# Performance work log

Hardware: AMD Instinct MI355X
Metric: run time of the kernel (lower is better)

## Reference

```python
import jax, jax.numpy as jnp
import numpy as np

EMBED_DIM = 1024
HEADS = 16
HEAD_DIM = EMBED_DIM // HEADS


def setup_inputs() -> dict:
    key = jax.random.key(0)
    ks = jax.random.split(key, 5)
    B, N, C = 2, 2048, EMBED_DIM
    scale = 1.0 / np.sqrt(C)
    x = jax.random.normal(ks[0], (B, N, C), dtype=jnp.float32)
    W_qkv = jax.random.normal(ks[1], (C, 3 * C), dtype=jnp.float32) * scale
    b_qkv = jax.random.normal(ks[2], (3 * C,), dtype=jnp.float32) * 0.01
    W_out = jax.random.normal(ks[3], (C, C), dtype=jnp.float32) * scale
    b_out = jax.random.normal(ks[4], (C,), dtype=jnp.float32) * 0.01
    return {"x": x, "W_qkv": W_qkv, "b_qkv": b_qkv, "W_out": W_out, "b_out": b_out}


def reference(x, W_qkv, b_qkv, W_out, b_out):
    B, N, C = x.shape
    qkv = x @ W_qkv + b_qkv                      # [B, N, 3C]
    qkv = qkv.reshape(B, N, 3, HEADS, HEAD_DIM)
    qkv = jnp.transpose(qkv, (2, 0, 3, 1, 4))    # [3, B, H, N, d]
    q, k, v = qkv[0], qkv[1], qkv[2]
    attn = jnp.einsum('bhnd,bhmd->bhnm', q, k) / np.sqrt(HEAD_DIM)
    attn = jax.nn.softmax(attn, axis=-1)
    out = jnp.einsum('bhnm,bhmd->bhnd', attn, v)  # [B, H, N, d]
    out = jnp.transpose(out, (0, 2, 1, 3)).reshape(B, N, C)
    return out @ W_out + b_out
```

## Files before the change

kernel.cpp:

```cpp
#include <hip/hip_runtime.h>
#include <stdint.h>

typedef __bf16 bf16_t;
typedef bf16_t bf16x8 __attribute__((ext_vector_type(8)));
typedef bf16_t bf16x2v __attribute__((ext_vector_type(2)));
typedef float f32x4 __attribute__((ext_vector_type(4)));
typedef float f32x16 __attribute__((ext_vector_type(16)));
typedef uint32_t u32x2 __attribute__((ext_vector_type(2)));
typedef uint32_t u32x4 __attribute__((ext_vector_type(4)));

#define BATCH 2
#define SEQ 2048
#define CDIM 1024
#define NH 16
#define HD 64

#define QSCALE 0.18033688011f

__device__ __forceinline__ uint16_t f32_bf16(float f) {
    __bf16 h = (__bf16)f;
    return __builtin_bit_cast(uint16_t, h);
}

__device__ __forceinline__ uint32_t pack_bf16(float a, float b) {
    bf16x2v t;
    t.x = (__bf16)a;
    t.y = (__bf16)b;
    return __builtin_bit_cast(uint32_t, t);
}

__device__ __forceinline__ bf16x8 ld8(const uint16_t* p) {
    return *reinterpret_cast<const bf16x8*>(p);
}

__device__ __forceinline__ void swap32(uint32_t& a, uint32_t& b) {
#if __has_builtin(__builtin_amdgcn_permlane32_swap)
    u32x2 r = __builtin_amdgcn_permlane32_swap(a, b, false, false);
    a = r.x;
    b = r.y;
#else
    asm("v_permlane32_swap_b32 %0, %1" : "+v"(a), "+v"(b));
#endif
}

__device__ __forceinline__ void gld16(const uint16_t* g, uint16_t* l) {
    __builtin_amdgcn_global_load_lds(
        (__attribute__((address_space(1))) void*)(g),
        (__attribute__((address_space(3))) void*)(l), 16, 0, 0);
}

#define LDS_FENCE() asm volatile("s_waitcnt lgkmcnt(0)" ::: "memory")

__global__ __launch_bounds__(256) void prep_kernel(
        const float* __restrict__ x, uint16_t* __restrict__ x_bf,
        const float* __restrict__ Wqkv, uint16_t* __restrict__ wqkvT,
        const float* __restrict__ Wout, uint16_t* __restrict__ woutT) {
    const int bid = blockIdx.x, tid = threadIdx.x;
    if (bid < 4096) {
        int i = (bid * 256 + tid) * 4;
        float4 v = *(const float4*)(x + i);
        ushort4 o;
        o.x = f32_bf16(v.x);
        o.y = f32_bf16(v.y);
        o.z = f32_bf16(v.z);
        o.w = f32_bf16(v.w);
        *(ushort4*)(x_bf + i) = o;
        return;
    }
    __shared__ float tile[32][33];
    const float* in;
    uint16_t* outp;
    int idx, Cc, ncx;
    if (bid < 4096 + 3072) { idx = bid - 4096; in = Wqkv; outp = wqkvT; Cc = 3072; ncx = 96; }
    else                   { idx = bid - 7168; in = Wout; outp = woutT; Cc = 1024; ncx = 32; }
    const int R = 1024;
    int bx = idx % ncx, by = idx / ncx;
    int c0 = bx * 32, r0 = by * 32;
    int tx = tid & 31, ty = tid >> 5;
#pragma unroll
    for (int i = 0; i < 4; i++)
        tile[ty + i * 8][tx] = in[(size_t)(r0 + ty + i * 8) * Cc + c0 + tx];
    __syncthreads();
    const int rr = tid >> 3, seg = tid & 7;
    ushort4 o;
    o.x = f32_bf16(tile[seg * 4 + 0][rr]);
    o.y = f32_bf16(tile[seg * 4 + 1][rr]);
    o.z = f32_bf16(tile[seg * 4 + 2][rr]);
    o.w = f32_bf16(tile[seg * 4 + 3][rr]);
    *(ushort4*)(outp + (size_t)(c0 + rr) * R + r0 + seg * 4) = o;
}

template <int BM, int BN, int MODE>
__global__ __launch_bounds__(256) void gemm_t(
        const uint16_t* __restrict__ A, const uint16_t* __restrict__ Bt, int K,
        const float* __restrict__ bias,
        uint16_t* __restrict__ qw, uint16_t* __restrict__ kw, uint16_t* __restrict__ vt,
        float* __restrict__ out) {
    constexpr int WT_M = BM / 2, WT_N = BN / 2;
    constexpr int MI = WT_M / 16, NJ = WT_N / 16;
    constexpr int ASEG_W = BM / 64, BSEG_W = BN / 64;
    constexpr int AB = 2 * BM * 32 + 2 * BN * 32;
    constexpr int TS = (MODE == 0) ? 4 * 64 * 68 : 0;
    constexpr int SM = AB > TS ? AB : TS;
    __shared__ uint16_t smem[SM];
    uint16_t* As = smem;
    uint16_t* Bs = smem + 2 * BM * 32;

    const int m0 = blockIdx.y * BM, n0 = blockIdx.x * BN;
    const int tid = threadIdx.x;
    const int w = tid >> 6, lane = tid & 63;
    const int quad = lane >> 4, l16 = lane & 15;
    const int wm = (w >> 1) * WT_M, wn = (w & 1) * WT_N;

    const int srow = lane >> 2;
    const int schunk = (lane & 3) ^ (srow & 3);

    const uint16_t* aP[ASEG_W];
    const uint16_t* bP[BSEG_W];
    int aL[ASEG_W], bL[BSEG_W];
#pragma unroll
    for (int s = 0; s < ASEG_W; s++) {
        int seg = w * ASEG_W + s;
        aP[s] = A + (size_t)(m0 + seg * 16 + srow) * K + schunk * 8;
        aL[s] = seg * 512;
    }
#pragma unroll
    for (int s = 0; s < BSEG_W; s++) {
        int seg = w * BSEG_W + s;
        bP[s] = Bt + (size_t)(n0 + seg * 16 + srow) * K + schunk * 8;
        bL[s] = seg * 512;
    }

    auto stage = [&](int buf, int k0) {
#pragma unroll
        for (int s = 0; s < ASEG_W; s++) gld16(aP[s] + k0, As + buf * BM * 32 + aL[s]);
#pragma unroll
        for (int s = 0; s < BSEG_W; s++) gld16(bP[s] + k0, Bs + buf * BN * 32 + bL[s]);
    };

    const int cslot = (quad ^ (l16 & 3)) * 8;
    f32x4 acc[MI][NJ] = {};

    stage(0, 0);
    const int iters = K / 32;
    for (int it = 0; it < iters; ++it) {
        __syncthreads();
        if (it + 1 < iters) stage((it + 1) & 1, (it + 1) * 32);
        const uint16_t* A_ = As + (it & 1) * BM * 32;
        const uint16_t* B_ = Bs + (it & 1) * BN * 32;
        bf16x8 af[MI], bfr[NJ];
#pragma unroll
        for (int i = 0; i < MI; i++) af[i] = ld8(&A_[(wm + i * 16 + l16) * 32 + cslot]);
#pragma unroll
        for (int j = 0; j < NJ; j++) bfr[j] = ld8(&B_[(wn + j * 16 + l16) * 32 + cslot]);
#pragma unroll
        for (int i = 0; i < MI; i++)
#pragma unroll
            for (int j = 0; j < NJ; j++)
                acc[i][j] = __builtin_amdgcn_mfma_f32_16x16x32_bf16(af[i], bfr[j], acc[i][j], 0, 0, 0);
    }

    const int nbase = n0 + wn;
    float bj[NJ];
#pragma unroll
    for (int j = 0; j < NJ; j++) bj[j] = bias[nbase + j * 16 + l16];

    if constexpr (MODE == 1) {
#pragma unroll
        for (int j = 0; j < NJ; j++) {
#pragma unroll
            for (int i = 0; i < MI; i++)
#pragma unroll
                for (int r = 0; r < 4; r++) {
                    int m = m0 + wm + i * 16 + quad * 4 + r;
                    out[(size_t)m * CDIM + nbase + j * 16 + l16] = acc[i][j][r] + bj[j];
                }
        }
    } else {
        __syncthreads();
        uint16_t* T = smem + w * 64 * 68;
        const int gmb = m0 + wm;
        const int b = gmb >> 11, ns0 = gmb & 2047;

        if (nbase < 2048) {
            const int which = nbase >> 10, h = (nbase & 1023) >> 6;
            const float sc = (which == 0) ? QSCALE : 1.0f;
#pragma unroll
            for (int i = 0; i < 4; i++)
#pragma unroll
                for (int j = 0; j < 4; j++)
#pragma unroll
                    for (int r = 0; r < 4; r++)
                        T[(i * 16 + quad * 4 + r) * 68 + j * 16 + l16] =
                            f32_bf16((acc[i][j][r] + bj[j]) * sc);
            LDS_FENCE();
            uint16_t* dst = ((which == 0) ? qw : kw) +
                            (((size_t)b * NH + h) * SEQ + ns0 + lane) * HD;
#pragma unroll
            for (int g = 0; g < 8; g++) {
                bf16x8 v = ld8(&T[lane * 68 + g * 8]);
                *(bf16x8*)(dst + g * 8) = v;
            }
        } else {
#pragma unroll
            for (int i = 0; i < 4; i++)
#pragma unroll
                for (int j = 0; j < 4; j++) {
                    u32x2 pr;
                    pr.x = pack_bf16(acc[i][j][0] + bj[j], acc[i][j][1] + bj[j]);
                    pr.y = pack_bf16(acc[i][j][2] + bj[j], acc[i][j][3] + bj[j]);
                    *(u32x2*)&T[(j * 16 + l16) * 68 + i * 16 + quad * 4] = pr;
                }
            LDS_FENCE();
            const int h = (nbase - 2048) >> 6;
            uint16_t* dst = vt + (((size_t)b * NH + h) * HD + lane) * SEQ + ns0;
#pragma unroll
            for (int g = 0; g < 16; g++) {
                u32x2 d2 = *(const u32x2*)&T[lane * 68 + g * 4];
                *(u32x2*)(dst + g * 4) = d2;
            }
        }
    }
}

__global__ __launch_bounds__(256) void attn_kernel(
        const uint16_t* __restrict__ qg, const uint16_t* __restrict__ kg,
        const uint16_t* __restrict__ vt, uint16_t* __restrict__ og) {
    __shared__ uint16_t Ks[2][128 * 64];
    __shared__ uint16_t Vs[2][64 * 128];

    const int bh = blockIdx.x;
    const int qt = blockIdx.y;
    const int tid = threadIdx.x;
    const int w = tid >> 6, lane = tid & 63;
    const int l32 = lane & 31, hi = lane >> 5;
    const int qrow0 = qt * 128 + w * 32;
    const size_t base = (size_t)bh * SEQ * HD;

    bf16x8 qf[4];
#pragma unroll
    for (int s = 0; s < 4; s++)
        qf[s] = ld8(qg + base + (size_t)(qrow0 + l32) * HD + s * 16 + hi * 8);

    const int krow = lane >> 3;
    const int kch = (lane & 7) ^ krow;
    const int vrow = lane >> 4;
    const uint16_t* ksrc[4];
    const uint16_t* vsrc[4];
#pragma unroll
    for (int s = 0; s < 4; s++) {
        int seg = w * 4 + s;
        ksrc[s] = kg + base + (size_t)(seg * 8 + krow) * HD + kch * 8;
        int vd = seg * 4 + vrow;
        int vch = (lane & 15) ^ (vd & 15);
        vsrc[s] = vt + base + (size_t)vd * SEQ + vch * 8;
    }

    f32x16 o_acc[2] = {};
    float l_red = 0.0f;

    auto stage = [&](int buf) {
#pragma unroll
        for (int s = 0; s < 4; s++) {
            int seg = w * 4 + s;
            gld16(ksrc[s], &Ks[buf][seg * 512]);
            ksrc[s] += 128 * HD;
        }
#pragma unroll
        for (int s = 0; s < 4; s++) {
            int seg = w * 4 + s;
            gld16(vsrc[s], &Vs[buf][seg * 512]);
            vsrc[s] += 128;
        }
    };

    stage(0);

    const int kxe = l32 & 7;
    const int vxe = l32 & 15;
    const int krowb = l32 * 64;
    const int vrowb = l32 * 128;
    int kco[4];
#pragma unroll
    for (int s = 0; s < 4; s++) kco[s] = ((2 * s + hi) ^ kxe) * 8;
    int vco[4][2];
#pragma unroll
    for (int kvb = 0; kvb < 4; kvb++)
#pragma unroll
        for (int cp = 0; cp < 2; cp++)
            vco[kvb][cp] = ((kvb * 4 + cp * 2 + hi) ^ vxe) * 8;

    const f32x16 fzero = {};

    const int NT = SEQ / 128;
    for (int it = 0; it < NT; ++it) {
        __syncthreads();
        if (it + 1 < NT) stage((it + 1) & 1);
        const uint16_t* K_ = Ks[it & 1];
        const uint16_t* V_ = Vs[it & 1];

        bf16x8 kf[2][4];
        f32x16 S[2];
#pragma unroll
        for (int s = 0; s < 4; s++) kf[0][s] = ld8(K_ + krowb + kco[s]);
        S[0] = fzero;
#pragma unroll
        for (int s = 0; s < 4; s++)
            S[0] = __builtin_amdgcn_mfma_f32_32x32x16_bf16(kf[0][s], qf[s], S[0], 0, 0, 0);

#pragma unroll
        for (int kvb = 0; kvb < 4; kvb++) {
            const int cur = kvb & 1, nxt = cur ^ 1;

            if (kvb < 3) {
#pragma unroll
                for (int s = 0; s < 4; s++)
                    kf[nxt][s] = ld8(K_ + (kvb + 1) * 2048 + krowb + kco[s]);
            }
            bf16x8 vf[2][2];
#pragma unroll
            for (int cp = 0; cp < 2; cp++)
#pragma unroll
                for (int mf = 0; mf < 2; mf++)
                    vf[cp][mf] = ld8(V_ + vrowb + mf * 4096 + vco[kvb][cp]);

            float p[16];
#pragma unroll
            for (int i = 0; i < 16; i++) p[i] = __builtin_amdgcn_exp2f(S[cur][i]);
            {
                float s0 = (p[0] + p[1]) + (p[2] + p[3]);
                float s1 = (p[4] + p[5]) + (p[6] + p[7]);
                float s2 = (p[8] + p[9]) + (p[10] + p[11]);
                float s3 = (p[12] + p[13]) + (p[14] + p[15]);
                l_red += (s0 + s1) + (s2 + s3);
            }
            uint32_t pk0[4], pk1[4];
#pragma unroll
            for (int c = 0; c < 4; c++) {
                pk0[c] = pack_bf16(p[4 * c + 0], p[4 * c + 1]);
                pk1[c] = pack_bf16(p[4 * c + 2], p[4 * c + 3]);
            }

            if (kvb < 3) {
                S[nxt] = fzero;
#pragma unroll
                for (int s = 0; s < 4; s++)
                    S[nxt] = __builtin_amdgcn_mfma_f32_32x32x16_bf16(kf[nxt][s], qf[s], S[nxt], 0, 0, 0);
            }

#pragma unroll
            for (int cp = 0; cp < 2; cp++) {
                uint32_t b0 = pk0[2 * cp], b2 = pk0[2 * cp + 1];
                uint32_t b1 = pk1[2 * cp], b3 = pk1[2 * cp + 1];
                swap32(b0, b2);
                swap32(b1, b3);
                u32x4 t;
                t.x = b0; t.y = b1; t.z = b2; t.w = b3;
                bf16x8 pb = __builtin_bit_cast(bf16x8, t);
#pragma unroll
                for (int mf = 0; mf < 2; mf++)
                    o_acc[mf] = __builtin_amdgcn_mfma_f32_32x32x16_bf16(vf[cp][mf], pb, o_acc[mf], 0, 0, 0);
            }
        }
    }

    uint32_t la = __builtin_bit_cast(uint32_t, l_red), lb = la;
    swap32(la, lb);
    const float l_tot = __builtin_bit_cast(float, la) + __builtin_bit_cast(float, lb);
    const float inv = __builtin_amdgcn_rcpf(l_tot);

    const int b = bh >> 4, h = bh & 15;
    const int ns = qrow0 + l32;
    uint16_t* orow = og + (((size_t)b * SEQ + ns) * NH + h) * HD;
#pragma unroll
    for (int mf = 0; mf < 2; mf++)
#pragma unroll
        for (int c = 0; c < 4; c++) {
            u32x2 pr;
            pr.x = pack_bf16(o_acc[mf][4 * c + 0] * inv, o_acc[mf][4 * c + 1] * inv);
            pr.y = pack_bf16(o_acc[mf][4 * c + 2] * inv, o_acc[mf][4 * c + 3] * inv);
            *(u32x2*)(orow + mf * 32 + c * 8 + hi * 4) = pr;
        }
}

extern "C" void kernel_launch(void* const* d_in, const int* in_sizes, int n_in,
                              void* d_out, int out_size, void* d_ws, size_t ws_size,
                              hipStream_t stream) {
    const float* x = (const float*)d_in[0];
    const float* Wqkv = (const float*)d_in[1];
    const float* bqkv = (const float*)d_in[2];
    const float* Wout = (const float*)d_in[3];
    const float* bout = (const float*)d_in[4];
    float* out = (float*)d_out;

    uint16_t* ws = (uint16_t*)d_ws;
    uint16_t* x_bf  = ws;
    uint16_t* wqkvT = x_bf + 4194304;
    uint16_t* woutT = wqkvT + 3145728;
    uint16_t* qw    = woutT + 1048576;
    uint16_t* kw    = qw + 4194304;
    uint16_t* vtw   = kw + 4194304;
    uint16_t* attn  = vtw + 4194304;

    prep_kernel<<<8192, 256, 0, stream>>>(x, x_bf, Wqkv, wqkvT, Wout, woutT);

    gemm_t<128, 128, 0><<<dim3(24, 32), 256, 0, stream>>>(
        x_bf, wqkvT, 1024, bqkv, qw, kw, vtw, nullptr);

    attn_kernel<<<dim3(32, 16), 256, 0, stream>>>(qw, kw, vtw, attn);

    gemm_t<64, 128, 1><<<dim3(8, 64), 256, 0, stream>>>(
        attn, woutT, 1024, bout, nullptr, nullptr, nullptr, out);
}
```

Measured before the change: 183.6 us.

## Pipeline QK^T across KV tiles via global K prefetch and coalesce QKV stores

The attention loop now computes the first S block of the next KV tile during the current tile's last sub-block. It reads those K fragments straight from global memory, so the per-tile pipeline bubble after each barrier goes away. MFMA sections are wrapped in s_setprio to favour matrix issue. The QKV epilogue stores are reorganised so that eight lanes write contiguous 128-byte rows, which improves coalescing for the Q/K and transposed V outputs. The direct global K loads add latency and register pressure.

```diff
diff --git a/kernel.cpp b/kernel.cpp
--- a/kernel.cpp
+++ b/kernel.cpp
@@ -181,6 +181,7 @@
         uint16_t* T = smem + w * 64 * 68;
         const int gmb = m0 + wm;
         const int b = gmb >> 11, ns0 = gmb & 2047;
+        const int lrow = lane >> 3, lch = lane & 7;
 
         if (nbase < 2048) {
             const int which = nbase >> 10, h = (nbase & 1023) >> 6;
@@ -195,11 +196,12 @@
                             f32_bf16((acc[i][j][r] + bj[j]) * sc);
             LDS_FENCE();
             uint16_t* dst = ((which == 0) ? qw : kw) +
-                            (((size_t)b * NH + h) * SEQ + ns0 + lane) * HD;
+                            (((size_t)b * NH + h) * SEQ + ns0) * HD;
 #pragma unroll
             for (int g = 0; g < 8; g++) {
-                bf16x8 v = ld8(&T[lane * 68 + g * 8]);
-                *(bf16x8*)(dst + g * 8) = v;
+                int r = g * 8 + lrow;
+                bf16x8 v = ld8(&T[r * 68 + lch * 8]);
+                *(bf16x8*)(dst + (size_t)r * HD + lch * 8) = v;
             }
         } else {
 #pragma unroll
@@ -213,11 +215,12 @@
                 }
             LDS_FENCE();
             const int h = (nbase - 2048) >> 6;
-            uint16_t* dst = vt + (((size_t)b * NH + h) * HD + lane) * SEQ + ns0;
-#pragma unroll
-            for (int g = 0; g < 16; g++) {
-                u32x2 d2 = *(const u32x2*)&T[lane * 68 + g * 4];
-                *(u32x2*)(dst + g * 4) = d2;
+            uint16_t* dstb = vt + ((size_t)b * NH + h) * HD * SEQ + ns0;
+#pragma unroll
+            for (int g = 0; g < 8; g++) {
+                int dr = g * 8 + lrow;
+                bf16x8 v2 = ld8(&T[dr * 68 + lch * 8]);
+                *(bf16x8*)(dstb + (size_t)dr * SEQ + lch * 8) = v2;
             }
         }
     }
@@ -291,6 +294,20 @@
             vco[kvb][cp] = ((kvb * 4 + cp * 2 + hi) ^ vxe) * 8;
 
     const f32x16 fzero = {};
+    const uint16_t* kg_pref = kg + base + (size_t)l32 * HD + hi * 8;
+
+    f32x16 S[2];
+    {
+        bf16x8 k0[4];
+#pragma unroll
+        for (int s = 0; s < 4; s++) k0[s] = ld8(kg_pref + s * 16);
+        S[0] = fzero;
+        __builtin_amdgcn_s_setprio(1);
+#pragma unroll
+        for (int s = 0; s < 4; s++)
+            S[0] = __builtin_amdgcn_mfma_f32_32x32x16_bf16(k0[s], qf[s], S[0], 0, 0, 0);
+        __builtin_amdgcn_s_setprio(0);
+    }
 
     const int NT = SEQ / 128;
     for (int it = 0; it < NT; ++it) {
@@ -298,25 +315,24 @@
         if (it + 1 < NT) stage((it + 1) & 1);
         const uint16_t* K_ = Ks[it & 1];
         const uint16_t* V_ = Vs[it & 1];
-
-        bf16x8 kf[2][4];
-        f32x16 S[2];
-#pragma unroll
-        for (int s = 0; s < 4; s++) kf[0][s] = ld8(K_ + krowb + kco[s]);
-        S[0] = fzero;
-#pragma unroll
-        for (int s = 0; s < 4; s++)
-            S[0] = __builtin_amdgcn_mfma_f32_32x32x16_bf16(kf[0][s], qf[s], S[0], 0, 0, 0);
+        bf16x8 kf3[4];
 
 #pragma unroll
         for (int kvb = 0; kvb < 4; kvb++) {
             const int cur = kvb & 1, nxt = cur ^ 1;
 
+            bf16x8 kf[4];
             if (kvb < 3) {
 #pragma unroll
                 for (int s = 0; s < 4; s++)
-                    kf[nxt][s] = ld8(K_ + (kvb + 1) * 2048 + krowb + kco[s]);
-            }
+                    kf[s] = ld8(K_ + (kvb + 1) * 2048 + krowb + kco[s]);
+            }
+            if (kvb == 2 && it + 1 < NT) {
+                const uint16_t* kgp = kg_pref + (size_t)(it + 1) * (128 * HD);
+#pragma unroll
+                for (int s = 0; s < 4; s++) kf3[s] = ld8(kgp + s * 16);
+            }
+
             bf16x8 vf[2][2];
 #pragma unroll
             for (int cp = 0; cp < 2; cp++)
@@ -341,11 +357,17 @@
                 pk1[c] = pack_bf16(p[4 * c + 2], p[4 * c + 3]);
             }
 
+            __builtin_amdgcn_s_setprio(1);
             if (kvb < 3) {
                 S[nxt] = fzero;
 #pragma unroll
                 for (int s = 0; s < 4; s++)
-                    S[nxt] = __builtin_amdgcn_mfma_f32_32x32x16_bf16(kf[nxt][s], qf[s], S[nxt], 0, 0, 0);
+                    S[nxt] = __builtin_amdgcn_mfma_f32_32x32x16_bf16(kf[s], qf[s], S[nxt], 0, 0, 0);
+            } else if (it + 1 < NT) {
+                S[nxt] = fzero;
+#pragma unroll
+                for (int s = 0; s < 4; s++)
+                    S[nxt] = __builtin_amdgcn_mfma_f32_32x32x16_bf16(kf3[s], qf[s], S[nxt], 0, 0, 0);
             }
 
 #pragma unroll
@@ -361,6 +383,7 @@
                 for (int mf = 0; mf < 2; mf++)
                     o_acc[mf] = __builtin_amdgcn_mfma_f32_32x32x16_bf16(vf[cp][mf], pb, o_acc[mf], 0, 0, 0);
             }
+            __builtin_amdgcn_s_setprio(0);
         }
     }
 
```

Measured after the change: 186.9 us. Within noise of the previous version (+1.8%).
